# Performance work log

Measured on AMD Instinct MI355X. Metric: run time of the kernel, lower is better.

## Reference

```python
import jax, jax.numpy as jnp
import numpy as np

U = 128  # linear_units

def setup_inputs() -> dict:
    key = jax.random.key(0)
    k1, k2, k3, k4, k5, k6 = jax.random.split(key, 6)
    B, S, D = 16, 2048, 128
    x = jax.random.normal(k1, (B, S, D), dtype=jnp.float32)
    t = jax.random.uniform(k2, (B, S), dtype=jnp.float32)
    # glorot_uniform inits
    lim_qk = np.sqrt(6.0 / (D + U)).astype(np.float32)
    Wq = jax.random.uniform(k3, (D, U), minval=-lim_qk, maxval=lim_qk, dtype=jnp.float32)
    Wk = jax.random.uniform(k4, (D, U), minval=-lim_qk, maxval=lim_qk, dtype=jnp.float32)
    lim_s = np.sqrt(6.0 / (1 + S)).astype(np.float32)
    theta = jax.random.uniform(k5, (1, S), minval=-lim_s, maxval=lim_s, dtype=jnp.float32)
    mu = jax.random.uniform(k6, (1, S), minval=-lim_s, maxval=lim_s, dtype=jnp.float32)
    return {"x": x, "t": t, "Wq": Wq, "Wk": Wk, "theta": theta, "mu": mu}

def reference(x, t, Wq, Wk, theta, mu):
    # x: (B,S,D), t: (B,S), theta/mu: (1,S)
    scale = jnp.sqrt(jnp.asarray(U, dtype=x.dtype))
    q = x @ Wq                                   # (B,S,U)
    k = x @ Wk                                   # (B,S,U)
    scores = jnp.einsum('biu,bju->bij', q, k) / scale  # (B,S,S)
    alphas = jax.nn.softmax(scores, axis=-1)
    gn = jnp.einsum('bij,bjd->bid', alphas, x)   # weighted sum == alphas @ x, (B,S,D)
    time_fact = jax.nn.sigmoid(theta - mu * t)   # (B,S)
    v = jnp.sum(gn * time_fact[:, :, None], axis=1)  # (B,D)
    return v
```

## Files before the change

kernel.cpp:

```cpp
#include <hip/hip_runtime.h>
#include <hip/hip_bf16.h>

#define SS 2048
#define DD 128
#define BB 16
#define LDST 136
#define SCT 268

typedef short bf16x8 __attribute__((ext_vector_type(8)));
typedef float f32x4 __attribute__((ext_vector_type(4)));
typedef unsigned short ushort_t;

__device__ __forceinline__ unsigned short f2bf(float f) {
  union { float f; unsigned u; } v; v.f = f;
  unsigned r = v.u + 0x7fffu + ((v.u >> 16) & 1u);
  return (unsigned short)(r >> 16);
}
__device__ __forceinline__ float fexp2(float x) { return __builtin_amdgcn_exp2f(x); }


__global__ __launch_bounds__(256) void wprep(
    const float* __restrict__ Wq, const float* __restrict__ Wk,
    ushort_t* __restrict__ wt_g) {
  int idx = blockIdx.x * 256 + threadIdx.x;
  int r = idx & 16383, uu = r >> 7, d = r & 127;
  if (idx < 16384)
    wt_g[uu * 128 + d] = f2bf(Wq[d * 128 + uu] * 0.1275174346f);
  else
    wt_g[(uu + 128) * 128 + d] = f2bf(Wk[d * 128 + uu]);
}

__global__ __launch_bounds__(256, 2) void qk_gemm(
    const float* __restrict__ x, const ushort_t* __restrict__ wt_g,
    uint4* __restrict__ qF, uint4* __restrict__ kF) {
  __shared__ ushort_t xs[64 * LDST];
  __shared__ ushort_t sc[64 * SCT];
  const int tid = threadIdx.x, wave = tid >> 6, lane = tid & 63;
  const int lq = lane & 15, quad = lane >> 4;
  const int m0 = blockIdx.x * 64;

#pragma unroll
  for (int i = 0; i < 8; ++i) {
    int idx = i * 256 + tid;
    int row = idx >> 5, c4 = (idx & 31) * 4;
    const float4 v = *(const float4*)(x + (size_t)(m0 + row) * DD + c4);
    ushort4 h;
    h.x = f2bf(v.x); h.y = f2bf(v.y); h.z = f2bf(v.z); h.w = f2bf(v.w);
    *(ushort4*)(&xs[row * LDST + c4]) = h;
  }
  bf16x8 wf[4][4];
#pragma unroll
  for (int nt = 0; nt < 4; ++nt)
#pragma unroll
    for (int ks = 0; ks < 4; ++ks)
      wf[nt][ks] = *(const bf16x8*)(wt_g + (wave * 64 + nt * 16 + lq) * 128 + ks * 32 + quad * 8);
  __syncthreads();

  f32x4 acc[4][4];
#pragma unroll
  for (int mt = 0; mt < 4; ++mt)
#pragma unroll
    for (int nt = 0; nt < 4; ++nt) acc[mt][nt] = (f32x4){0.f, 0.f, 0.f, 0.f};
#pragma unroll
  for (int mt = 0; mt < 4; ++mt) {
    bf16x8 af[4];
#pragma unroll
    for (int ks = 0; ks < 4; ++ks)
      af[ks] = *(const bf16x8*)(&xs[(mt * 16 + lq) * LDST + ks * 32 + quad * 8]);
#pragma unroll
    for (int nt = 0; nt < 4; ++nt)
#pragma unroll
      for (int ks = 0; ks < 4; ++ks)
        acc[mt][nt] = __builtin_amdgcn_mfma_f32_16x16x32_bf16(af[ks], wf[nt][ks], acc[mt][nt], 0, 0, 0);
  }
#pragma unroll
  for (int mt = 0; mt < 4; ++mt)
#pragma unroll
    for (int nt = 0; nt < 4; ++nt)
#pragma unroll
      for (int r = 0; r < 4; ++r)
        sc[(mt * 16 + quad * 4 + r) * SCT + wave * 64 + nt * 16 + lq] = f2bf(acc[mt][nt][r]);
  __syncthreads();
#pragma unroll
  for (int i = 0; i < 8; ++i) {
    int c = i * 256 + tid;
    int lane_c = c & 63, ks_c = (c >> 6) & 3, g_c = (c >> 8) & 3, isk = c >> 10;
    int li = lane_c & 15, qd = lane_c >> 4;
    int col = isk * 128 + ks_c * 32 + qd * 8;
    uint4 v = *(const uint4*)(&sc[(g_c * 16 + li) * SCT + col]);
    size_t G = (size_t)blockIdx.x * 4 + g_c;
    uint4* dst = isk ? kF : qF;
    dst[(G * 4 + ks_c) * 64 + lane_c] = v;
  }
}

__global__ __launch_bounds__(256, 2) void attn_fused(
    const uint4* __restrict__ qF, const uint4* __restrict__ kF,
    const float* __restrict__ t, const float* __restrict__ theta,
    const float* __restrict__ mu, float* __restrict__ w) {
  const int b = blockIdx.x >> 5;
  const int ib = blockIdx.x & 31;
  const int i0 = ib * 64;
  const int tid = threadIdx.x, wave = tid >> 6, lane = tid & 63;
  const int lq = lane & 15, quad = lane >> 4;

  __shared__ float rs_lds[4][64];
  __shared__ float c_lds[64];

  const bf16x8* qc = (const bf16x8*)qF;
  const bf16x8* kc = (const bf16x8*)kF;

  bf16x8 af[4][4];
#pragma unroll
  for (int mt = 0; mt < 4; ++mt)
#pragma unroll
    for (int ks = 0; ks < 4; ++ks)
      af[mt][ks] = qc[((size_t)(b * 128 + ib * 4 + mt) * 4 + ks) * 64 + lane];

  const bf16x8* kb = kc + (size_t)b * 128 * 4 * 64 + lane;
  auto loadg = [&](bf16x8 (&f)[4], int g) {
#pragma unroll
    for (int ks = 0; ks < 4; ++ks)
      f[ks] = kb[((size_t)g * 4 + ks) * 64];
  };

  const f32x4 z4 = {0.f, 0.f, 0.f, 0.f};
  auto mfma16 = [&](f32x4 (&acc)[4], bf16x8 (&f)[4]) {
    __builtin_amdgcn_s_setprio(1);
#pragma unroll
    for (int mt = 0; mt < 4; ++mt)
      acc[mt] = __builtin_amdgcn_mfma_f32_16x16x32_bf16(af[mt][0], f[0], z4, 0, 0, 0);
#pragma unroll
    for (int ks = 1; ks < 4; ++ks)
#pragma unroll
      for (int mt = 0; mt < 4; ++mt)
        acc[mt] = __builtin_amdgcn_mfma_f32_16x16x32_bf16(af[mt][ks], f[ks], acc[mt], 0, 0, 0);
    __builtin_amdgcn_s_setprio(0);
  };

  float rowsum[4][4];
#pragma unroll
  for (int mt = 0; mt < 4; ++mt)
#pragma unroll
    for (int r = 0; r < 4; ++r) rowsum[mt][r] = 0.f;

  auto proc1 = [&](f32x4 (&acc)[4]) {
#pragma unroll
    for (int mt = 0; mt < 4; ++mt)
#pragma unroll
      for (int r = 0; r < 4; ++r) rowsum[mt][r] += fexp2(acc[mt][r]);
  };

  const int gw = wave * 2;
  bf16x8 f0[4], f1[4];
  f32x4 a0[4], a1[4];

  loadg(f0, gw);
  loadg(f1, gw + 1);
  mfma16(a0, f0);
  for (int jt = 0; jt < 15; ++jt) {
    loadg(f0, gw + (jt + 1) * 8);
    mfma16(a1, f1);
    proc1(a0);
    loadg(f1, gw + (jt + 1) * 8 + 1);
    mfma16(a0, f0);
    proc1(a1);
  }
  mfma16(a1, f1);
  proc1(a0);
  proc1(a1);

#pragma unroll
  for (int d2 = 1; d2 <= 8; d2 <<= 1)
#pragma unroll
    for (int mt = 0; mt < 4; ++mt)
#pragma unroll
      for (int r = 0; r < 4; ++r)
        rowsum[mt][r] += __shfl_xor(rowsum[mt][r], d2, 64);
  if (lq == 0) {
#pragma unroll
    for (int mt = 0; mt < 4; ++mt)
#pragma unroll
      for (int r = 0; r < 4; ++r)
        rs_lds[wave][mt * 16 + quad * 4 + r] = rowsum[mt][r];
  }
  __syncthreads();
  if (tid < 64) {
    float l = rs_lds[0][tid] + rs_lds[1][tid] + rs_lds[2][tid] + rs_lds[3][tid];
    int gi = i0 + tid;
    float z = theta[gi] - mu[gi] * t[b * SS + gi];
    float tf = 1.f / (1.f + fexp2(-z * 1.44269504f));
    c_lds[tid] = tf / l;
  }
  __syncthreads();
  float creg[4][4];
#pragma unroll
  for (int mt = 0; mt < 4; ++mt)
#pragma unroll
    for (int r = 0; r < 4; ++r) creg[mt][r] = c_lds[mt * 16 + quad * 4 + r];

  auto proc2 = [&](f32x4 (&acc)[4], int g) {
    float cs = 0.f;
#pragma unroll
    for (int mt = 0; mt < 4; ++mt)
#pragma unroll
      for (int r = 0; r < 4; ++r) cs = fmaf(creg[mt][r], fexp2(acc[mt][r]), cs);
    cs += __shfl_xor(cs, 16, 64);
    cs += __shfl_xor(cs, 32, 64);
    if (lane < 16) atomicAdd(&w[b * SS + g * 16 + lane], cs);
  };

  loadg(f0, gw);
  loadg(f1, gw + 1);
  mfma16(a0, f0);
  for (int jt = 0; jt < 15; ++jt) {
    loadg(f0, gw + (jt + 1) * 8);
    mfma16(a1, f1);
    proc2(a0, gw + jt * 8);
    loadg(f1, gw + (jt + 1) * 8 + 1);
    mfma16(a0, f0);
    proc2(a1, gw + jt * 8 + 1);
  }
  mfma16(a1, f1);
  proc2(a0, gw + 15 * 8);
  proc2(a1, gw + 15 * 8 + 1);
}

__global__ __launch_bounds__(256) void finalize(
    const float* __restrict__ x, const float* __restrict__ w,
    float* __restrict__ out) {
  const int b = blockIdx.x >> 5;
  const int j0 = (blockIdx.x & 31) * 64;
  const int tid = threadIdx.x;
  const int d = tid & 127, jo = tid >> 7;
  float acc = 0.f;
  for (int jj = 0; jj < 32; ++jj) {
    int j = j0 + jj * 2 + jo;
    acc = fmaf(w[b * SS + j], x[((size_t)b * SS + j) * DD + d], acc);
  }
  __shared__ float red[256];
  red[tid] = acc;
  __syncthreads();
  if (tid < 128) atomicAdd(&out[b * DD + tid], red[tid] + red[tid + 128]);
}

extern "C" void kernel_launch(void* const* d_in, const int* in_sizes, int n_in,
                              void* d_out, int out_size, void* d_ws, size_t ws_size,
                              hipStream_t stream) {
  const float* x = (const float*)d_in[0];
  const float* t = (const float*)d_in[1];
  const float* Wq = (const float*)d_in[2];
  const float* Wk = (const float*)d_in[3];
  const float* theta = (const float*)d_in[4];
  const float* mu = (const float*)d_in[5];
  float* out = (float*)d_out;

  uint4* qF = (uint4*)d_ws;
  uint4* kF = qF + (size_t)2048 * 4 * 64;
  ushort_t* wt_g = (ushort_t*)(kF + (size_t)2048 * 4 * 64);
  float* w = (float*)(wt_g + 256 * 128);

  hipMemsetAsync(w, 0, (size_t)BB * SS * sizeof(float), stream);
  hipMemsetAsync(d_out, 0, (size_t)BB * DD * sizeof(float), stream);

  wprep<<<dim3(128), dim3(256), 0, stream>>>(Wq, Wk, wt_g);
  qk_gemm<<<dim3(512), dim3(256), 0, stream>>>(x, wt_g, qF, kF);
  attn_fused<<<dim3(512), dim3(256), 0, stream>>>(qF, kF, t, theta, mu, w);
  finalize<<<dim3(512), dim3(256), 0, stream>>>(x, w, out);
}
```

Measured before the change: 128.3 us.

## Remap attention blocks per XCD, pipeline K loads with explicit waits, vectorize finalize

Assigns attention blocks so that each batch's K fragments stay on one XCD, which should improve L2 reuse. The two S-sweeps now use a single accumulator with double-buffered K fragment loads, with explicit vmcnt waits and sched barriers so MFMA work overlaps the next loads. The finalize kernel switches to float4 loads of x and a tree reduction in LDS. The risk is that the hand-placed waits and barriers constrain the compiler's scheduling, and the single accumulator serializes MFMA and exp work.

```diff
diff --git a/kernel.cpp b/kernel.cpp
--- a/kernel.cpp
+++ b/kernel.cpp
@@ -10,6 +10,9 @@
 typedef short bf16x8 __attribute__((ext_vector_type(8)));
 typedef float f32x4 __attribute__((ext_vector_type(4)));
 typedef unsigned short ushort_t;
+
+#define SB0() __builtin_amdgcn_sched_barrier(0)
+#define WAITV(n) asm volatile("s_waitcnt vmcnt(" #n ")" ::: "memory")
 
 __device__ __forceinline__ unsigned short f2bf(float f) {
   union { float f; unsigned u; } v; v.f = f;
@@ -98,8 +101,9 @@
     const uint4* __restrict__ qF, const uint4* __restrict__ kF,
     const float* __restrict__ t, const float* __restrict__ theta,
     const float* __restrict__ mu, float* __restrict__ w) {
-  const int b = blockIdx.x >> 5;
-  const int ib = blockIdx.x & 31;
+  const int xcd = blockIdx.x & 7, s = blockIdx.x >> 3;
+  const int b = xcd + ((s >> 5) << 3);
+  const int ib = s & 31;
   const int i0 = ib * 64;
   const int tid = threadIdx.x, wave = tid >> 6, lane = tid & 63;
   const int lq = lane & 15, quad = lane >> 4;
@@ -108,7 +112,6 @@
   __shared__ float c_lds[64];
 
   const bf16x8* qc = (const bf16x8*)qF;
-  const bf16x8* kc = (const bf16x8*)kF;
 
   bf16x8 af[4][4];
 #pragma unroll
@@ -117,24 +120,25 @@
     for (int ks = 0; ks < 4; ++ks)
       af[mt][ks] = qc[((size_t)(b * 128 + ib * 4 + mt) * 4 + ks) * 64 + lane];
 
-  const bf16x8* kb = kc + (size_t)b * 128 * 4 * 64 + lane;
+  const bf16x8* kb = (const bf16x8*)kF + (size_t)b * 128 * 4 * 64 + lane;
   auto loadg = [&](bf16x8 (&f)[4], int g) {
 #pragma unroll
     for (int ks = 0; ks < 4; ++ks)
       f[ks] = kb[((size_t)g * 4 + ks) * 64];
   };
+  auto G = [&](int m) { return (m >> 1) * 8 + wave * 2 + (m & 1); };
 
   const f32x4 z4 = {0.f, 0.f, 0.f, 0.f};
-  auto mfma16 = [&](f32x4 (&acc)[4], bf16x8 (&f)[4]) {
+  auto mfma16 = [&](f32x4 (&a)[4], bf16x8 (&f)[4]) {
     __builtin_amdgcn_s_setprio(1);
 #pragma unroll
     for (int mt = 0; mt < 4; ++mt)
-      acc[mt] = __builtin_amdgcn_mfma_f32_16x16x32_bf16(af[mt][0], f[0], z4, 0, 0, 0);
+      a[mt] = __builtin_amdgcn_mfma_f32_16x16x32_bf16(af[mt][0], f[0], z4, 0, 0, 0);
 #pragma unroll
     for (int ks = 1; ks < 4; ++ks)
 #pragma unroll
       for (int mt = 0; mt < 4; ++mt)
-        acc[mt] = __builtin_amdgcn_mfma_f32_16x16x32_bf16(af[mt][ks], f[ks], acc[mt], 0, 0, 0);
+        a[mt] = __builtin_amdgcn_mfma_f32_16x16x32_bf16(af[mt][ks], f[ks], a[mt], 0, 0, 0);
     __builtin_amdgcn_s_setprio(0);
   };
 
@@ -143,32 +147,30 @@
   for (int mt = 0; mt < 4; ++mt)
 #pragma unroll
     for (int r = 0; r < 4; ++r) rowsum[mt][r] = 0.f;
-
-  auto proc1 = [&](f32x4 (&acc)[4]) {
-#pragma unroll
-    for (int mt = 0; mt < 4; ++mt)
-#pragma unroll
-      for (int r = 0; r < 4; ++r) rowsum[mt][r] += fexp2(acc[mt][r]);
-  };
-
-  const int gw = wave * 2;
-  bf16x8 f0[4], f1[4];
-  f32x4 a0[4], a1[4];
-
-  loadg(f0, gw);
-  loadg(f1, gw + 1);
-  mfma16(a0, f0);
-  for (int jt = 0; jt < 15; ++jt) {
-    loadg(f0, gw + (jt + 1) * 8);
-    mfma16(a1, f1);
-    proc1(a0);
-    loadg(f1, gw + (jt + 1) * 8 + 1);
-    mfma16(a0, f0);
-    proc1(a1);
-  }
-  mfma16(a1, f1);
-  proc1(a0);
-  proc1(a1);
+  auto proc1 = [&](f32x4 (&a)[4]) {
+#pragma unroll
+    for (int mt = 0; mt < 4; ++mt)
+#pragma unroll
+      for (int r = 0; r < 4; ++r) rowsum[mt][r] += fexp2(a[mt][r]);
+  };
+
+  bf16x8 fA[4], fB[4];
+  f32x4 a[4];
+
+  loadg(fA, G(0));
+  loadg(fB, G(1));
+  for (int m = 0; m < 30; m += 2) {
+    WAITV(4); SB0();
+    mfma16(a, fA);
+    loadg(fA, G(m + 2)); SB0();
+    proc1(a);
+    WAITV(4); SB0();
+    mfma16(a, fB);
+    loadg(fB, G(m + 3)); SB0();
+    proc1(a);
+  }
+  WAITV(4); SB0(); mfma16(a, fA); SB0(); proc1(a);
+  WAITV(0); SB0(); mfma16(a, fB); SB0(); proc1(a);
 
 #pragma unroll
   for (int d2 = 1; d2 <= 8; d2 <<= 1)
@@ -199,31 +201,31 @@
 #pragma unroll
     for (int r = 0; r < 4; ++r) creg[mt][r] = c_lds[mt * 16 + quad * 4 + r];
 
-  auto proc2 = [&](f32x4 (&acc)[4], int g) {
+  auto proc2 = [&](f32x4 (&aa)[4], int g) {
     float cs = 0.f;
 #pragma unroll
     for (int mt = 0; mt < 4; ++mt)
 #pragma unroll
-      for (int r = 0; r < 4; ++r) cs = fmaf(creg[mt][r], fexp2(acc[mt][r]), cs);
+      for (int r = 0; r < 4; ++r) cs = fmaf(creg[mt][r], fexp2(aa[mt][r]), cs);
     cs += __shfl_xor(cs, 16, 64);
     cs += __shfl_xor(cs, 32, 64);
     if (lane < 16) atomicAdd(&w[b * SS + g * 16 + lane], cs);
   };
 
-  loadg(f0, gw);
-  loadg(f1, gw + 1);
-  mfma16(a0, f0);
-  for (int jt = 0; jt < 15; ++jt) {
-    loadg(f0, gw + (jt + 1) * 8);
-    mfma16(a1, f1);
-    proc2(a0, gw + jt * 8);
-    loadg(f1, gw + (jt + 1) * 8 + 1);
-    mfma16(a0, f0);
-    proc2(a1, gw + jt * 8 + 1);
-  }
-  mfma16(a1, f1);
-  proc2(a0, gw + 15 * 8);
-  proc2(a1, gw + 15 * 8 + 1);
+  loadg(fA, G(0));
+  loadg(fB, G(1));
+  for (int m = 0; m < 30; m += 2) {
+    WAITV(4); SB0();
+    mfma16(a, fA);
+    loadg(fA, G(m + 2)); SB0();
+    proc2(a, G(m));
+    WAITV(4); SB0();
+    mfma16(a, fB);
+    loadg(fB, G(m + 3)); SB0();
+    proc2(a, G(m + 1));
+  }
+  WAITV(4); SB0(); mfma16(a, fA); SB0(); proc2(a, G(30));
+  WAITV(0); SB0(); mfma16(a, fB); SB0(); proc2(a, G(31));
 }
 
 __global__ __launch_bounds__(256) void finalize(
@@ -232,16 +234,41 @@
   const int b = blockIdx.x >> 5;
   const int j0 = (blockIdx.x & 31) * 64;
   const int tid = threadIdx.x;
-  const int d = tid & 127, jo = tid >> 7;
-  float acc = 0.f;
-  for (int jj = 0; jj < 32; ++jj) {
-    int j = j0 + jj * 2 + jo;
-    acc = fmaf(w[b * SS + j], x[((size_t)b * SS + j) * DD + d], acc);
-  }
-  __shared__ float red[256];
+  const int d4 = (tid & 31) * 4, jo = tid >> 5;
+  float4 a0 = {0.f, 0.f, 0.f, 0.f}, a1 = {0.f, 0.f, 0.f, 0.f};
+#pragma unroll
+  for (int jj = 0; jj < 4; ++jj) {
+    int ja = j0 + jj * 16 + jo, jb = ja + 8;
+    float wa = w[b * SS + ja], wb = w[b * SS + jb];
+    const float4 xa = *(const float4*)(x + ((size_t)b * SS + ja) * DD + d4);
+    const float4 xb = *(const float4*)(x + ((size_t)b * SS + jb) * DD + d4);
+    a0.x = fmaf(wa, xa.x, a0.x); a0.y = fmaf(wa, xa.y, a0.y);
+    a0.z = fmaf(wa, xa.z, a0.z); a0.w = fmaf(wa, xa.w, a0.w);
+    a1.x = fmaf(wb, xb.x, a1.x); a1.y = fmaf(wb, xb.y, a1.y);
+    a1.z = fmaf(wb, xb.z, a1.z); a1.w = fmaf(wb, xb.w, a1.w);
+  }
+  __shared__ float4 red[256];
+  float4 acc = {a0.x + a1.x, a0.y + a1.y, a0.z + a1.z, a0.w + a1.w};
   red[tid] = acc;
   __syncthreads();
-  if (tid < 128) atomicAdd(&out[b * DD + tid], red[tid] + red[tid + 128]);
+  if (tid < 128) {
+    float4 o = red[tid + 128];
+    red[tid].x += o.x; red[tid].y += o.y; red[tid].z += o.z; red[tid].w += o.w;
+  }
+  __syncthreads();
+  if (tid < 64) {
+    float4 o = red[tid + 64];
+    red[tid].x += o.x; red[tid].y += o.y; red[tid].z += o.z; red[tid].w += o.w;
+  }
+  __syncthreads();
+  if (tid < 32) {
+    float4 v = red[tid], o = red[tid + 32];
+    v.x += o.x; v.y += o.y; v.z += o.z; v.w += o.w;
+    atomicAdd(&out[b * DD + d4 + 0], v.x);
+    atomicAdd(&out[b * DD + d4 + 1], v.y);
+    atomicAdd(&out[b * DD + d4 + 2], v.z);
+    atomicAdd(&out[b * DD + d4 + 3], v.w);
+  }
 }
 
 extern "C" void kernel_launch(void* const* d_in, const int* in_sizes, int n_in,
```

Result: no change. 127.2 us (-0.8%).
